# Kernel optimization log

Measured on AMD Instinct MI355X. Metric: run time of the kernel, lower is better.

The kernel has to match this reference:

```python
import jax, jax.numpy as jnp
import numpy as np

N_NODES = 50000
N_EDGES = 800000
D = 128
N_LAYERS = 3
BN_EPS = 1e-5


def setup_inputs() -> dict:
    key = jax.random.key(0)
    k1, k2, k3, k4 = jax.random.split(key, 4)
    feat = jax.random.normal(k1, (N_NODES, D), dtype=jnp.float32)
    src = jax.random.randint(k2, (N_EDGES,), 0, N_NODES, dtype=jnp.int64)
    dst = jax.random.randint(k3, (N_EDGES,), 0, N_NODES, dtype=jnp.int64)
    Ws = jax.random.normal(k4, (N_LAYERS, D, D), dtype=jnp.float32) * (1.0 / np.sqrt(D))
    bs = jnp.zeros((N_LAYERS, D), dtype=jnp.float32)
    gammas = jnp.ones((N_LAYERS - 1, D), dtype=jnp.float32)
    betas = jnp.zeros((N_LAYERS - 1, D), dtype=jnp.float32)
    return {"feat": feat, "src": src, "dst": dst, "Ws": Ws, "bs": bs,
            "gammas": gammas, "betas": betas}


def _degrees(src, dst, n_nodes, dtype):
    ones = jnp.ones(src.shape, dtype=dtype)
    deg_out = jax.ops.segment_sum(ones, src, num_segments=n_nodes)
    deg_in = jax.ops.segment_sum(ones, dst, num_segments=n_nodes)
    # DGL clamps zero degrees to 1
    return jnp.maximum(deg_out, 1.0), jnp.maximum(deg_in, 1.0)


def _graph_conv(h, src, dst, W, b, norm_src, norm_dst):
    # GraphConv(norm='both'): D_in^{-1/2} * A^T * (D_out^{-1/2} * h) @ W + b
    h = h * norm_src[:, None]          # scale source features by out-degree norm
    h = h @ W                          # dense transform (in == out dims)
    agg = jax.ops.segment_sum(h[src], dst, num_segments=h.shape[0])  # SpMM
    return agg * norm_dst[:, None] + b


def _batchnorm(h, gamma, beta):
    mean = jnp.mean(h, axis=0)
    var = jnp.mean(jnp.square(h - mean), axis=0)  # biased var (training forward)
    return gamma * (h - mean) * jax.lax.rsqrt(var + BN_EPS) + beta


def reference(feat, src, dst, Ws, bs, gammas, betas):
    n_nodes = feat.shape[0]
    deg_out, deg_in = _degrees(src, dst, n_nodes, feat.dtype)
    norm_src = jax.lax.rsqrt(deg_out)
    norm_dst = jax.lax.rsqrt(deg_in)
    h = feat
    for i in range(N_LAYERS):
        h = _graph_conv(h, src, dst, Ws[i], bs[i], norm_src, norm_dst)
        if i < N_LAYERS - 1:
            h = _batchnorm(h, gammas[i], betas[i])
            h = jax.nn.relu(h)
            # dropout p=0.0 -> identity
    return h
```

## Files before the change

### kernel.cpp

```cpp
#include <hip/hip_runtime.h>
#include <stdint.h>

#define DD 128
#define EPS 1e-5f

static __device__ __forceinline__ void fma4(float4& a, float s, const float4& w){
  a.x = fmaf(s, w.x, a.x); a.y = fmaf(s, w.y, a.y);
  a.z = fmaf(s, w.z, a.z); a.w = fmaf(s, w.w, a.w);
}

static __device__ __forceinline__ unsigned short f2bf(float x){
  unsigned u = __float_as_uint(x);
  return (unsigned short)((u + 0x7FFFu + ((u >> 16) & 1u)) >> 16);
}
#define BFLO(v) __uint_as_float(((v) & 0xFFFFu) << 16)
#define BFHI(v) __uint_as_float((v) & 0xFFFF0000u)

__global__ __launch_bounds__(256) void degree_kernel(const int* __restrict__ src, const int* __restrict__ dst,
                                                     int* __restrict__ deg_out, int* __restrict__ deg_in, int ne){
  int e = blockIdx.x*256 + threadIdx.x;
  if (e < ne){
    atomicAdd(&deg_out[src[e]], 1);
    atomicAdd(&deg_in[dst[e]], 1);
  }
}

__global__ __launch_bounds__(256) void norm_kernel(const int* __restrict__ deg_out, const int* __restrict__ deg_in,
                                                   float* __restrict__ ns, float* __restrict__ nd, int n){
  int i = blockIdx.x*256 + threadIdx.x;
  if (i < n){
    int dout = deg_out[i] > 1 ? deg_out[i] : 1;
    int din  = deg_in[i]  > 1 ? deg_in[i]  : 1;
    ns[i] = rsqrtf((float)dout);
    nd[i] = rsqrtf((float)din);
  }
}

__global__ __launch_bounds__(1024) void scan_kernel(const int* __restrict__ counts, int* __restrict__ rowptr, int n){
  __shared__ int wsum[16];
  __shared__ int sbase, snext;
  int t = threadIdx.x, lane = t & 63, w = t >> 6;
  if (t == 0) sbase = 0;
  __syncthreads();
  int ntiles = (n + 1023) >> 10;
  for (int tile = 0; tile < ntiles; tile++){
    int i = (tile << 10) + t;
    int v = (i < n) ? counts[i] : 0;
    int x = v;
    #pragma unroll
    for (int off = 1; off < 64; off <<= 1){
      int u = __shfl_up(x, off);
      if (lane >= off) x += u;
    }
    if (lane == 63) wsum[w] = x;
    __syncthreads();
    if (t == 0){
      int acc = 0;
      #pragma unroll
      for (int k2 = 0; k2 < 16; k2++){ int s = wsum[k2]; wsum[k2] = acc; acc += s; }
      snext = sbase + acc;
    }
    __syncthreads();
    int excl = sbase + wsum[w] + x - v;
    if (i < n) rowptr[i] = excl;
    if (i == n - 1) rowptr[n] = excl + v;
    __syncthreads();
    if (t == 0) sbase = snext;
    __syncthreads();
  }
}

__global__ __launch_bounds__(256) void fill_kernel(const int* __restrict__ src, const int* __restrict__ dst,
                                                   const int* __restrict__ rowptr, int* __restrict__ cursor,
                                                   int* __restrict__ csr_src, int ne){
  int e = blockIdx.x*256 + threadIdx.x;
  if (e < ne){
    int d = dst[e];
    int pos = rowptr[d] + atomicAdd(&cursor[d], 1);
    csr_src[pos] = src[e];
  }
}

__global__ __launch_bounds__(256) void gemm_kernel(
    const float* __restrict__ hin, const float* __restrict__ W,
    const float* __restrict__ nsrc, const float* __restrict__ ss, int has_ss,
    unsigned short* __restrict__ hout, int nrows)
{
  __shared__ __align__(16) float lw[64*DD];
  __shared__ __align__(16) float ht[DD*36];
  __shared__ float lsc[DD], lsh[DD];
  int t = threadIdx.x;
  if (t < DD){
    lsc[t] = has_ss ? ss[t]      : 1.0f;
    lsh[t] = has_ss ? ss[DD + t] : 0.0f;
  }
  {
    const float4* W4 = (const float4*)W;
    float4* lw4 = (float4*)lw;
    #pragma unroll
    for (int i = 0; i < 8; i++) lw4[i*256 + t] = W4[i*256 + t];
  }
  __syncthreads();

  int base = blockIdx.x * 32;
  #pragma unroll
  for (int i = 0; i < 16; i++){
    int idx = i*256 + t;
    int r = idx >> 7, cc = idx & 127;
    int row = base + r;
    float v = 0.f;
    if (row < nrows){
      v = hin[(size_t)row*DD + cc];
      v = fmaf(v, lsc[cc], lsh[cc]);
      if (has_ss) v = fmaxf(v, 0.f);
      v *= nsrc[row];
    }
    ht[cc*36 + r] = v;
  }
  __syncthreads();

  int j = t & 31, g = t >> 5;
  float4 a0 = {0,0,0,0}, a1 = {0,0,0,0}, a2 = {0,0,0,0}, a3 = {0,0,0,0};
  #pragma unroll 8
  for (int k = 0; k < 64; k++){
    float4 hv = *(const float4*)&ht[k*36 + g*4];
    float4 wv = *(const float4*)&lw[k*DD + j*4];
    fma4(a0, hv.x, wv); fma4(a1, hv.y, wv); fma4(a2, hv.z, wv); fma4(a3, hv.w, wv);
  }
  __syncthreads();
  {
    const float4* W4 = (const float4*)W + 2048;
    float4* lw4 = (float4*)lw;
    #pragma unroll
    for (int i = 0; i < 8; i++) lw4[i*256 + t] = W4[i*256 + t];
  }
  __syncthreads();
  #pragma unroll 8
  for (int k = 64; k < 128; k++){
    float4 hv = *(const float4*)&ht[k*36 + g*4];
    float4 wv = *(const float4*)&lw[(k-64)*DD + j*4];
    fma4(a0, hv.x, wv); fma4(a1, hv.y, wv); fma4(a2, hv.z, wv); fma4(a3, hv.w, wv);
  }
  int r0 = base + g*4;
  ushort4 o;
  if (r0 + 0 < nrows){ o.x=f2bf(a0.x); o.y=f2bf(a0.y); o.z=f2bf(a0.z); o.w=f2bf(a0.w);
    ((ushort4*)hout)[(size_t)(r0+0)*32 + j] = o; }
  if (r0 + 1 < nrows){ o.x=f2bf(a1.x); o.y=f2bf(a1.y); o.z=f2bf(a1.z); o.w=f2bf(a1.w);
    ((ushort4*)hout)[(size_t)(r0+1)*32 + j] = o; }
  if (r0 + 2 < nrows){ o.x=f2bf(a2.x); o.y=f2bf(a2.y); o.z=f2bf(a2.z); o.w=f2bf(a2.w);
    ((ushort4*)hout)[(size_t)(r0+2)*32 + j] = o; }
  if (r0 + 3 < nrows){ o.x=f2bf(a3.x); o.y=f2bf(a3.y); o.z=f2bf(a3.z); o.w=f2bf(a3.w);
    ((ushort4*)hout)[(size_t)(r0+3)*32 + j] = o; }
}

__global__ __launch_bounds__(256) void agg_kernel(
    const unsigned short* __restrict__ h2, const int* __restrict__ rowptr,
    const int* __restrict__ csr_src, const float* __restrict__ ndst,
    const float* __restrict__ bias, float* __restrict__ hout,
    float* __restrict__ colsum, float* __restrict__ colsq,
    int do_stats, int nnodes)
{
  __shared__ float red[4][DD];
  int t = threadIdx.x;
  int lane = t & 63, w = t >> 6;
  int qid = lane >> 4, sub = lane & 15;
  int slot = blockIdx.x*4 + w, nslots = gridDim.x*4;
  const uint4* h4 = (const uint4*)h2;
  float bcol[8];
  #pragma unroll
  for (int k = 0; k < 8; k++) bcol[k] = bias[sub*8 + k];
  float s[8], q[8];
  #pragma unroll
  for (int k = 0; k < 8; k++){ s[k] = 0.f; q[k] = 0.f; }

  for (int node = slot; node < nnodes; node += nslots){
    int beg = rowptr[node], end = rowptr[node+1];
    int cnt = end - beg;
    float a[8];
    #pragma unroll
    for (int k = 0; k < 8; k++) a[k] = 0.f;
    for (int bse = 0; bse < cnt; bse += 64){
      int m = cnt - bse; if (m > 64) m = 64;
      int myidx = (bse + lane < cnt) ? csr_src[beg + bse + lane] : 0;
      #pragma unroll 4
      for (int jj = 0; jj < m; jj += 4){
        int e = jj + qid;
        int idx = __shfl(myidx, e);
        if (e < m){
          uint4 v = h4[(size_t)idx*16 + sub];
          a[0] += BFLO(v.x); a[1] += BFHI(v.x);
          a[2] += BFLO(v.y); a[3] += BFHI(v.y);
          a[4] += BFLO(v.z); a[5] += BFHI(v.z);
          a[6] += BFLO(v.w); a[7] += BFHI(v.w);
        }
      }
    }
    #pragma unroll
    for (int k = 0; k < 8; k++){
      a[k] += __shfl_xor(a[k], 16);
      a[k] += __shfl_xor(a[k], 32);
    }
    float ndv = ndst[node];
    float v[8];
    #pragma unroll
    for (int k = 0; k < 8; k++) v[k] = fmaf(a[k], ndv, bcol[k]);
    if (qid == 0){
      float4 o0, o1;
      o0.x = v[0]; o0.y = v[1]; o0.z = v[2]; o0.w = v[3];
      o1.x = v[4]; o1.y = v[5]; o1.z = v[6]; o1.w = v[7];
      *(float4*)&hout[(size_t)node*DD + sub*8]     = o0;
      *(float4*)&hout[(size_t)node*DD + sub*8 + 4] = o1;
      #pragma unroll
      for (int k = 0; k < 8; k++){ s[k] += v[k]; q[k] += v[k]*v[k]; }
    }
  }
  if (do_stats){
    if (qid == 0){
      #pragma unroll
      for (int k = 0; k < 8; k++) red[w][sub*8 + k] = s[k];
    }
    __syncthreads();
    if (t < DD) atomicAdd(&colsum[t], red[0][t] + red[1][t] + red[2][t] + red[3][t]);
    __syncthreads();
    if (qid == 0){
      #pragma unroll
      for (int k = 0; k < 8; k++) red[w][sub*8 + k] = q[k];
    }
    __syncthreads();
    if (t < DD) atomicAdd(&colsq[t], red[0][t] + red[1][t] + red[2][t] + red[3][t]);
  }
}

__global__ __launch_bounds__(DD) void bnfin_kernel(const float* __restrict__ colsum, const float* __restrict__ colsq,
                                                   const float* __restrict__ gamma, const float* __restrict__ beta,
                                                   float* __restrict__ ss, int n){
  int c = threadIdx.x;
  float invn = 1.0f / (float)n;
  float mean = colsum[c] * invn;
  float var  = colsq[c] * invn - mean*mean;
  var = fmaxf(var, 0.f);
  float sc = gamma[c] * rsqrtf(var + EPS);
  ss[c] = sc;
  ss[DD + c] = beta[c] - mean*sc;
}

extern "C" void kernel_launch(void* const* d_in, const int* in_sizes, int n_in,
                              void* d_out, int out_size, void* d_ws, size_t ws_size,
                              hipStream_t stream) {
  const float* feat   = (const float*)d_in[0];
  const int*   src    = (const int*)d_in[1];
  const int*   dst    = (const int*)d_in[2];
  const float* Ws     = (const float*)d_in[3];
  const float* bs     = (const float*)d_in[4];
  const float* gammas = (const float*)d_in[5];
  const float* betas  = (const float*)d_in[6];
  float* out = (float*)d_out;

  int n  = in_sizes[0] / DD;
  int ne = in_sizes[1];

  char* p = (char*)d_ws;
  int* deg_out = (int*)p; p += (size_t)n*sizeof(int);
  int* deg_in  = (int*)p; p += (size_t)n*sizeof(int);
  int* rowptr  = (int*)p; p += (size_t)(n+1)*sizeof(int);
  int* cursor  = (int*)p; p += (size_t)n*sizeof(int);
  int* csr_src = (int*)p; p += (size_t)ne*sizeof(int);
  float* ns      = (float*)p; p += (size_t)n*sizeof(float);
  float* nd      = (float*)p; p += (size_t)n*sizeof(float);
  float* colsum  = (float*)p; p += DD*sizeof(float);
  float* colsq   = (float*)p; p += DD*sizeof(float);
  float* scsh    = (float*)p; p += 2*DD*sizeof(float);
  p = (char*)(((uintptr_t)p + 255) & ~(uintptr_t)255);
  unsigned short* B0 = (unsigned short*)p; p += (size_t)n*DD*sizeof(unsigned short);

  hipMemsetAsync(deg_out, 0, 2*(size_t)n*sizeof(int), stream);
  degree_kernel<<<(ne+255)/256, 256, 0, stream>>>(src, dst, deg_out, deg_in, ne);
  norm_kernel<<<(n+255)/256, 256, 0, stream>>>(deg_out, deg_in, ns, nd, n);
  scan_kernel<<<1, 1024, 0, stream>>>(deg_in, rowptr, n);
  hipMemsetAsync(cursor, 0, (size_t)n*sizeof(int), stream);
  fill_kernel<<<(ne+255)/256, 256, 0, stream>>>(src, dst, rowptr, cursor, csr_src, ne);

  for (int L = 0; L < 3; L++){
    const float* hin = (L == 0) ? feat : out;
    gemm_kernel<<<(n+31)/32, 256, 0, stream>>>(hin, Ws + (size_t)L*DD*DD, ns, scsh, (L > 0) ? 1 : 0, B0, n);
    int do_stats = (L < 2) ? 1 : 0;
    if (do_stats) hipMemsetAsync(colsum, 0, 2*DD*sizeof(float), stream);
    agg_kernel<<<2048, 256, 0, stream>>>(B0, rowptr, csr_src, nd, bs + (size_t)L*DD, out,
                                         colsum, colsq, do_stats, n);
    if (do_stats) bnfin_kernel<<<1, DD, 0, stream>>>(colsum, colsq, gammas + (size_t)L*DD,
                                                     betas + (size_t)L*DD, scsh, n);
  }
}
```

Baseline: 580.2 us.

## Use bf16 MFMA for the dense transform with swizzled LDS tiles

Replaces the fp32 FMA outer-product GEMM with bf16 MFMA 16x16x32 instructions. W is converted to bf16 once per block and stored transposed in a XOR-swizzled LDS layout, and the input rows are also converted to bf16 in a swizzled layout. Each block now covers 64 rows instead of 32. This is meant to cut GEMM compute time, at the cost of rounding inputs and weights to bf16, which lowers precision, and of narrow 2-byte scattered output stores.

```diff
diff --git a/kernel.cpp b/kernel.cpp
--- a/kernel.cpp
+++ b/kernel.cpp
@@ -4,10 +4,8 @@
 #define DD 128
 #define EPS 1e-5f
 
-static __device__ __forceinline__ void fma4(float4& a, float s, const float4& w){
-  a.x = fmaf(s, w.x, a.x); a.y = fmaf(s, w.y, a.y);
-  a.z = fmaf(s, w.z, a.z); a.w = fmaf(s, w.w, a.w);
-}
+typedef short s8v __attribute__((ext_vector_type(8)));
+typedef float f4v __attribute__((ext_vector_type(4)));
 
 static __device__ __forceinline__ unsigned short f2bf(float x){
   unsigned u = __float_as_uint(x);
@@ -15,6 +13,10 @@
 }
 #define BFLO(v) __uint_as_float(((v) & 0xFFFFu) << 16)
 #define BFHI(v) __uint_as_float((v) & 0xFFFF0000u)
+
+static __device__ __forceinline__ int swzoff(int row, int k8){
+  return row*256 + ((k8 ^ (row & 7)) << 4);
+}
 
 __global__ __launch_bounds__(256) void degree_kernel(const int* __restrict__ src, const int* __restrict__ dst,
                                                      int* __restrict__ deg_out, int* __restrict__ deg_in, int ne){
@@ -86,71 +88,93 @@
     const float* __restrict__ nsrc, const float* __restrict__ ss, int has_ss,
     unsigned short* __restrict__ hout, int nrows)
 {
-  __shared__ __align__(16) float lw[64*DD];
-  __shared__ __align__(16) float ht[DD*36];
+  __shared__ __align__(16) unsigned short w_lds[DD*DD];
+  __shared__ __align__(16) unsigned short h_lds[64*DD];
   __shared__ float lsc[DD], lsh[DD];
   int t = threadIdx.x;
   if (t < DD){
     lsc[t] = has_ss ? ss[t]      : 1.0f;
     lsh[t] = has_ss ? ss[DD + t] : 0.0f;
   }
+  __syncthreads();
+
   {
-    const float4* W4 = (const float4*)W;
-    float4* lw4 = (float4*)lw;
-    #pragma unroll
-    for (int i = 0; i < 8; i++) lw4[i*256 + t] = W4[i*256 + t];
+    int c = t >> 1, khalf = t & 1;
+    char* wb = (char*)w_lds;
+    #pragma unroll
+    for (int i8 = 0; i8 < 8; i8++){
+      int k0 = khalf*64 + i8*8;
+      unsigned short o[8];
+      #pragma unroll
+      for (int j = 0; j < 8; j++) o[j] = f2bf(W[(size_t)(k0+j)*DD + c]);
+      uint4 pv;
+      pv.x = (unsigned)o[0] | ((unsigned)o[1] << 16);
+      pv.y = (unsigned)o[2] | ((unsigned)o[3] << 16);
+      pv.z = (unsigned)o[4] | ((unsigned)o[5] << 16);
+      pv.w = (unsigned)o[6] | ((unsigned)o[7] << 16);
+      *(uint4*)(wb + swzoff(c, khalf*8 + i8)) = pv;
+    }
+  }
+  int mbase = blockIdx.x * 64;
+  {
+    char* hb = (char*)h_lds;
+    #pragma unroll
+    for (int i = 0; i < 4; i++){
+      int s = i*256 + t;
+      int row = s >> 4, k8 = s & 15;
+      int grow = mbase + row;
+      uint4 pv = {0,0,0,0};
+      if (grow < nrows){
+        float4 p0 = *(const float4*)&hin[(size_t)grow*DD + k8*8];
+        float4 p1 = *(const float4*)&hin[(size_t)grow*DD + k8*8 + 4];
+        float nsv = nsrc[grow];
+        float vv[8] = {p0.x,p0.y,p0.z,p0.w,p1.x,p1.y,p1.z,p1.w};
+        unsigned short o[8];
+        #pragma unroll
+        for (int j = 0; j < 8; j++){
+          int col = k8*8 + j;
+          float v = fmaf(vv[j], lsc[col], lsh[col]);
+          if (has_ss) v = fmaxf(v, 0.f);
+          o[j] = f2bf(v * nsv);
+        }
+        pv.x = (unsigned)o[0] | ((unsigned)o[1] << 16);
+        pv.y = (unsigned)o[2] | ((unsigned)o[3] << 16);
+        pv.z = (unsigned)o[4] | ((unsigned)o[5] << 16);
+        pv.w = (unsigned)o[6] | ((unsigned)o[7] << 16);
+      }
+      *(uint4*)(hb + swzoff(row, k8)) = pv;
+    }
   }
   __syncthreads();
 
-  int base = blockIdx.x * 32;
-  #pragma unroll
-  for (int i = 0; i < 16; i++){
-    int idx = i*256 + t;
-    int r = idx >> 7, cc = idx & 127;
-    int row = base + r;
-    float v = 0.f;
-    if (row < nrows){
-      v = hin[(size_t)row*DD + cc];
-      v = fmaf(v, lsc[cc], lsh[cc]);
-      if (has_ss) v = fmaxf(v, 0.f);
-      v *= nsrc[row];
-    }
-    ht[cc*36 + r] = v;
-  }
-  __syncthreads();
-
-  int j = t & 31, g = t >> 5;
-  float4 a0 = {0,0,0,0}, a1 = {0,0,0,0}, a2 = {0,0,0,0}, a3 = {0,0,0,0};
-  #pragma unroll 8
-  for (int k = 0; k < 64; k++){
-    float4 hv = *(const float4*)&ht[k*36 + g*4];
-    float4 wv = *(const float4*)&lw[k*DD + j*4];
-    fma4(a0, hv.x, wv); fma4(a1, hv.y, wv); fma4(a2, hv.z, wv); fma4(a3, hv.w, wv);
-  }
-  __syncthreads();
-  {
-    const float4* W4 = (const float4*)W + 2048;
-    float4* lw4 = (float4*)lw;
-    #pragma unroll
-    for (int i = 0; i < 8; i++) lw4[i*256 + t] = W4[i*256 + t];
-  }
-  __syncthreads();
-  #pragma unroll 8
-  for (int k = 64; k < 128; k++){
-    float4 hv = *(const float4*)&ht[k*36 + g*4];
-    float4 wv = *(const float4*)&lw[(k-64)*DD + j*4];
-    fma4(a0, hv.x, wv); fma4(a1, hv.y, wv); fma4(a2, hv.z, wv); fma4(a3, hv.w, wv);
-  }
-  int r0 = base + g*4;
-  ushort4 o;
-  if (r0 + 0 < nrows){ o.x=f2bf(a0.x); o.y=f2bf(a0.y); o.z=f2bf(a0.z); o.w=f2bf(a0.w);
-    ((ushort4*)hout)[(size_t)(r0+0)*32 + j] = o; }
-  if (r0 + 1 < nrows){ o.x=f2bf(a1.x); o.y=f2bf(a1.y); o.z=f2bf(a1.z); o.w=f2bf(a1.w);
-    ((ushort4*)hout)[(size_t)(r0+1)*32 + j] = o; }
-  if (r0 + 2 < nrows){ o.x=f2bf(a2.x); o.y=f2bf(a2.y); o.z=f2bf(a2.z); o.w=f2bf(a2.w);
-    ((ushort4*)hout)[(size_t)(r0+2)*32 + j] = o; }
-  if (r0 + 3 < nrows){ o.x=f2bf(a3.x); o.y=f2bf(a3.y); o.z=f2bf(a3.z); o.w=f2bf(a3.w);
-    ((ushort4*)hout)[(size_t)(r0+3)*32 + j] = o; }
+  int lane = t & 63, w = t >> 6;
+  int lrow = lane & 15, lgrp = lane >> 4;
+  f4v acc[8];
+  #pragma unroll
+  for (int ct = 0; ct < 8; ct++) acc[ct] = (f4v){0.f,0.f,0.f,0.f};
+  const char* hb = (const char*)h_lds;
+  const char* wb = (const char*)w_lds;
+  #pragma unroll
+  for (int ks = 0; ks < 4; ks++){
+    int k8 = ks*4 + lgrp;
+    int arow = w*16 + lrow;
+    s8v a = *(const s8v*)(hb + swzoff(arow, k8));
+    #pragma unroll
+    for (int ct = 0; ct < 8; ct++){
+      int bcol = ct*16 + lrow;
+      s8v b = *(const s8v*)(wb + swzoff(bcol, k8));
+      acc[ct] = __builtin_amdgcn_mfma_f32_16x16x32_bf16(a, b, acc[ct], 0, 0, 0);
+    }
+  }
+  #pragma unroll
+  for (int ct = 0; ct < 8; ct++){
+    #pragma unroll
+    for (int r = 0; r < 4; r++){
+      int grow = mbase + w*16 + lgrp*4 + r;
+      if (grow < nrows)
+        hout[(size_t)grow*DD + ct*16 + lrow] = f2bf(acc[ct][r]);
+    }
+  }
 }
 
 __global__ __launch_bounds__(256) void agg_kernel(
@@ -282,7 +306,7 @@
 
   for (int L = 0; L < 3; L++){
     const float* hin = (L == 0) ? feat : out;
-    gemm_kernel<<<(n+31)/32, 256, 0, stream>>>(hin, Ws + (size_t)L*DD*DD, ns, scsh, (L > 0) ? 1 : 0, B0, n);
+    gemm_kernel<<<(n+63)/64, 256, 0, stream>>>(hin, Ws + (size_t)L*DD*DD, ns, scsh, (L > 0) ? 1 : 0, B0, n);
     int do_stats = (L < 2) ? 1 : 0;
     if (do_stats) hipMemsetAsync(colsum, 0, 2*DD*sizeof(float), stream);
     agg_kernel<<<2048, 256, 0, stream>>>(B0, rowptr, csr_src, nd, bs + (size_t)L*DD, out,
```

Measured after the change: 523.6 us. 1.11x faster.
